# Performance work log

Hardware: AMD Instinct MI355X
Metric: run time of the kernel (lower is better)

The kernel has to match this reference:

```python
import jax, jax.numpy as jnp
import numpy as np

D = H = W = 128
NUM_STEPS = 7  # MONAI DVF2DDF default


def _base_grid(dtype):
    zz, yy, xx = jnp.meshgrid(jnp.arange(D, dtype=dtype),
                              jnp.arange(H, dtype=dtype),
                              jnp.arange(W, dtype=dtype), indexing='ij')
    return jnp.stack([zz, yy, xx], 0)  # [3,D,H,W] voxel coords


def _warp(img, ddf, mode):
    # img: [1,C,D,H,W], ddf: [1,3,D,H,W] in voxel units.
    # Equivalent to grid_sample(align_corners=True, padding='border'):
    # border padding == clamp the voxel-space sample coordinate to [0, dim-1].
    dtype = ddf.dtype
    coords = _base_grid(dtype) + ddf[0]
    lims = jnp.array([D - 1, H - 1, W - 1], dtype=dtype).reshape(3, 1, 1, 1)
    coords = jnp.clip(coords, 0.0, lims)
    vol = img[0]  # [C,D,H,W]
    if mode == 'nearest':
        zi, yi, xi = jnp.round(coords).astype(jnp.int32)
        return vol[:, zi, yi, xi][None]
    z, y, x = coords
    z0 = jnp.floor(z); y0 = jnp.floor(y); x0 = jnp.floor(x)
    wz = z - z0; wy = y - y0; wx = x - x0
    z0i = z0.astype(jnp.int32); y0i = y0.astype(jnp.int32); x0i = x0.astype(jnp.int32)
    z1i = jnp.minimum(z0i + 1, D - 1)
    y1i = jnp.minimum(y0i + 1, H - 1)
    x1i = jnp.minimum(x0i + 1, W - 1)
    g = lambda a, b, c: vol[:, a, b, c]  # [C,D,H,W] gather
    out = (g(z0i, y0i, x0i) * (1 - wz) * (1 - wy) * (1 - wx)
         + g(z0i, y0i, x1i) * (1 - wz) * (1 - wy) * wx
         + g(z0i, y1i, x0i) * (1 - wz) * wy * (1 - wx)
         + g(z0i, y1i, x1i) * (1 - wz) * wy * wx
         + g(z1i, y0i, x0i) * wz * (1 - wy) * (1 - wx)
         + g(z1i, y0i, x1i) * wz * (1 - wy) * wx
         + g(z1i, y1i, x0i) * wz * wy * (1 - wx)
         + g(z1i, y1i, x1i) * wz * wy * wx)
    return out[None]


def _dvf2ddf(dvf):
    # scaling-and-squaring integration of a stationary velocity field
    ddf = dvf / (2.0 ** NUM_STEPS)
    for _ in range(NUM_STEPS):
        ddf = ddf + _warp(ddf, ddf, 'bilinear')
    return ddf


def setup_inputs() -> dict:
    key = jax.random.key(0)
    k1, k2, k3, k4 = jax.random.split(key, 4)
    dvf = jax.random.normal(k1, (1, 3, D, H, W), dtype=jnp.float32) * 0.5
    moving_image = jax.random.uniform(k2, (1, 1, D, H, W), dtype=jnp.float32)
    fixed_image = jax.random.uniform(k3, (1, 1, D, H, W), dtype=jnp.float32)
    moving_label = jax.random.randint(k4, (1, 1, D, H, W), 0, 4).astype(jnp.float32)
    return {'dvf': dvf, 'moving_image': moving_image,
            'fixed_image': fixed_image, 'moving_label': moving_label}


def reference(dvf, moving_image, fixed_image, moving_label):
    ddf = _dvf2ddf(dvf)
    pred_image = _warp(moving_image, ddf, 'bilinear')
    pred_label = _warp(moving_label, ddf, 'nearest')
    return (ddf, pred_image, pred_label, dvf)
```

## Files before the change

### kernel.cpp

```cpp
#include <hip/hip_runtime.h>

#define DD 128
constexpr int NV = DD * DD * DD;
constexpr float SCALE = 1.0f / 128.0f;

__device__ __forceinline__ int swizzle_block(int b) {
    return (b & 7) * 1024 + (b >> 3);
}

__device__ __forceinline__ void unpack_zyx(int tid, int& z, int& y, int& x) {
    x = tid & (DD - 1);
    y = (tid >> 7) & (DD - 1);
    z = tid >> 14;
}

__device__ __forceinline__ float clampc(float v) {
    return fminf(fmaxf(v, 0.0f), (float)(DD - 1));
}

struct Corners {
    int i000, i001, i010, i011, i100, i101, i110, i111;
    float w000, w001, w010, w011, w100, w101, w110, w111;
};

__device__ __forceinline__ Corners corner_setup(float cz, float cy, float cx) {
    float z0f = floorf(cz), y0f = floorf(cy), x0f = floorf(cx);
    float wz = cz - z0f, wy = cy - y0f, wx = cx - x0f;
    int z0 = (int)z0f, y0 = (int)y0f, x0 = (int)x0f;
    int z1 = min(z0 + 1, DD - 1);
    int y1 = min(y0 + 1, DD - 1);
    int x1 = min(x0 + 1, DD - 1);
    float omz = 1.0f - wz, omy = 1.0f - wy, omx = 1.0f - wx;
    int zs0 = z0 << 14, zs1 = z1 << 14;
    int ys0 = y0 << 7,  ys1 = y1 << 7;
    Corners c;
    c.i000 = zs0 + ys0 + x0; c.i001 = zs0 + ys0 + x1;
    c.i010 = zs0 + ys1 + x0; c.i011 = zs0 + ys1 + x1;
    c.i100 = zs1 + ys0 + x0; c.i101 = zs1 + ys0 + x1;
    c.i110 = zs1 + ys1 + x0; c.i111 = zs1 + ys1 + x1;
    c.w000 = omz * omy * omx; c.w001 = omz * omy * wx;
    c.w010 = omz * wy * omx;  c.w011 = omz * wy * wx;
    c.w100 = wz * omy * omx;  c.w101 = wz * omy * wx;
    c.w110 = wz * wy * omx;   c.w111 = wz * wy * wx;
    return c;
}

__device__ __forceinline__ void trilerp3i(const float* __restrict__ src,
                                          const Corners& c,
                                          float& r0, float& r1, float& r2) {
    const float* p000 = src + 3 * c.i000; const float* p001 = src + 3 * c.i001;
    const float* p010 = src + 3 * c.i010; const float* p011 = src + 3 * c.i011;
    const float* p100 = src + 3 * c.i100; const float* p101 = src + 3 * c.i101;
    const float* p110 = src + 3 * c.i110; const float* p111 = src + 3 * c.i111;
    r0 = c.w000*p000[0] + c.w001*p001[0] + c.w010*p010[0] + c.w011*p011[0]
       + c.w100*p100[0] + c.w101*p101[0] + c.w110*p110[0] + c.w111*p111[0];
    r1 = c.w000*p000[1] + c.w001*p001[1] + c.w010*p010[1] + c.w011*p011[1]
       + c.w100*p100[1] + c.w101*p101[1] + c.w110*p110[1] + c.w111*p111[1];
    r2 = c.w000*p000[2] + c.w001*p001[2] + c.w010*p010[2] + c.w011*p011[2]
       + c.w100*p100[2] + c.w101*p101[2] + c.w110*p110[2] + c.w111*p111[2];
}

__global__ __launch_bounds__(256)
void step1_kernel(const float* __restrict__ dvf, float* __restrict__ dst) {
    int b = swizzle_block(blockIdx.x);
    int tid = b * 256 + threadIdx.x;
    int z, y, x;
    unpack_zyx(tid, z, y, x);

    float d0 = dvf[tid] * SCALE;
    float d1 = dvf[tid + NV] * SCALE;
    float d2 = dvf[tid + 2 * NV] * SCALE;

    Corners c = corner_setup(clampc((float)z + d0),
                             clampc((float)y + d1),
                             clampc((float)x + d2));

    float r0 = 0.f, r1 = 0.f, r2 = 0.f;
    {
        const float* s0 = dvf;
        const float* s1 = dvf + NV;
        const float* s2 = dvf + 2 * NV;
        r0 = c.w000*s0[c.i000] + c.w001*s0[c.i001] + c.w010*s0[c.i010] + c.w011*s0[c.i011]
           + c.w100*s0[c.i100] + c.w101*s0[c.i101] + c.w110*s0[c.i110] + c.w111*s0[c.i111];
        r1 = c.w000*s1[c.i000] + c.w001*s1[c.i001] + c.w010*s1[c.i010] + c.w011*s1[c.i011]
           + c.w100*s1[c.i100] + c.w101*s1[c.i101] + c.w110*s1[c.i110] + c.w111*s1[c.i111];
        r2 = c.w000*s2[c.i000] + c.w001*s2[c.i001] + c.w010*s2[c.i010] + c.w011*s2[c.i011]
           + c.w100*s2[c.i100] + c.w101*s2[c.i101] + c.w110*s2[c.i110] + c.w111*s2[c.i111];
    }

    float* p = dst + 3 * tid;
    p[0] = d0 + r0 * SCALE;
    p[1] = d1 + r1 * SCALE;
    p[2] = d2 + r2 * SCALE;
}

__global__ __launch_bounds__(256)
void step_kernel(const float* __restrict__ src, float* __restrict__ dst) {
    int b = swizzle_block(blockIdx.x);
    int tid = b * 256 + threadIdx.x;
    int z, y, x;
    unpack_zyx(tid, z, y, x);

    const float* s = src + 3 * tid;
    float d0 = s[0], d1 = s[1], d2 = s[2];

    Corners c = corner_setup(clampc((float)z + d0),
                             clampc((float)y + d1),
                             clampc((float)x + d2));
    float r0, r1, r2;
    trilerp3i(src, c, r0, r1, r2);

    float* p = dst + 3 * tid;
    p[0] = d0 + r0; p[1] = d1 + r1; p[2] = d2 + r2;
}

__global__ __launch_bounds__(256)
void step7_final_kernel(const float* __restrict__ src,
                        const float* __restrict__ mimg,
                        const float* __restrict__ mlab,
                        float* __restrict__ ddf_out,
                        float* __restrict__ pred_img,
                        float* __restrict__ pred_lab) {
    int b = swizzle_block(blockIdx.x);
    int tid = b * 256 + threadIdx.x;
    int z, y, x;
    unpack_zyx(tid, z, y, x);

    const float* s = src + 3 * tid;
    float d0 = s[0], d1 = s[1], d2 = s[2];

    Corners c = corner_setup(clampc((float)z + d0),
                             clampc((float)y + d1),
                             clampc((float)x + d2));
    float r0, r1, r2;
    trilerp3i(src, c, r0, r1, r2);

    r0 += d0; r1 += d1; r2 += d2;
    ddf_out[tid]          = r0;
    ddf_out[tid + NV]     = r1;
    ddf_out[tid + 2 * NV] = r2;

    float cz = clampc((float)z + r0);
    float cy = clampc((float)y + r1);
    float cx = clampc((float)x + r2);

    {
        Corners g = corner_setup(cz, cy, cx);
        float v = g.w000*mimg[g.i000] + g.w001*mimg[g.i001]
                + g.w010*mimg[g.i010] + g.w011*mimg[g.i011]
                + g.w100*mimg[g.i100] + g.w101*mimg[g.i101]
                + g.w110*mimg[g.i110] + g.w111*mimg[g.i111];
        pred_img[tid] = v;
    }
    {
        int zi = (int)rintf(cz);
        int yi = (int)rintf(cy);
        int xi = (int)rintf(cx);
        pred_lab[tid] = mlab[(zi << 14) + (yi << 7) + xi];
    }
}

__global__ __launch_bounds__(256)
void copy_dvf_kernel(const float4* __restrict__ dvf, float4* __restrict__ dvf_out) {
    int tid = blockIdx.x * blockDim.x + threadIdx.x;
    dvf_out[tid] = dvf[tid];
}

extern "C" void kernel_launch(void* const* d_in, const int* in_sizes, int n_in,
                              void* d_out, int out_size, void* d_ws, size_t ws_size,
                              hipStream_t stream) {
    const float* dvf  = (const float*)d_in[0];
    const float* mimg = (const float*)d_in[1];
    const float* mlab = (const float*)d_in[3];

    float* out      = (float*)d_out;
    float* ddf_out  = out;
    float* pred_img = out + 3 * NV;
    float* pred_lab = out + 4 * NV;
    float* dvf_out  = out + 5 * NV;

    float* A = dvf_out;
    float* B = ddf_out;

    dim3 block(256);
    dim3 grid(NV / 256);

    step1_kernel<<<grid, block, 0, stream>>>(dvf, B);
    step_kernel<<<grid, block, 0, stream>>>(B, A);
    step_kernel<<<grid, block, 0, stream>>>(A, B);
    step_kernel<<<grid, block, 0, stream>>>(B, A);
    step_kernel<<<grid, block, 0, stream>>>(A, B);
    step_kernel<<<grid, block, 0, stream>>>(B, A);
    step7_final_kernel<<<grid, block, 0, stream>>>(A, mimg, mlab,
                                                   ddf_out, pred_img, pred_lab);
    copy_dvf_kernel<<<3 * NV / (4 * 256), block, 0, stream>>>(
        (const float4*)dvf, (float4*)dvf_out);
}
```

Before: 267.8 us.

## Pad displacement field to float4 for single-load vectorized trilinear gathers

```diff
diff --git a/kernel.cpp b/kernel.cpp
--- a/kernel.cpp
+++ b/kernel.cpp
@@ -3,10 +3,6 @@
 #define DD 128
 constexpr int NV = DD * DD * DD;
 constexpr float SCALE = 1.0f / 128.0f;
-
-__device__ __forceinline__ int swizzle_block(int b) {
-    return (b & 7) * 1024 + (b >> 3);
-}
 
 __device__ __forceinline__ void unpack_zyx(int tid, int& z, int& y, int& x) {
     x = tid & (DD - 1);
@@ -45,6 +41,105 @@
     return c;
 }
 
+
+__global__ __launch_bounds__(256)
+void pack_kernel(const float* __restrict__ dvf, float4* __restrict__ dst) {
+    int tid = blockIdx.x * blockDim.x + threadIdx.x;
+    float4 v;
+    v.x = dvf[tid] * SCALE;
+    v.y = dvf[tid + NV] * SCALE;
+    v.z = dvf[tid + 2 * NV] * SCALE;
+    v.w = 0.0f;
+    dst[tid] = v;
+}
+
+__global__ __launch_bounds__(256)
+void step4_kernel(const float4* __restrict__ src, float4* __restrict__ dst) {
+    int tid = blockIdx.x * blockDim.x + threadIdx.x;
+    int z, y, x;
+    unpack_zyx(tid, z, y, x);
+
+    float4 s = src[tid];
+
+    Corners c = corner_setup(clampc((float)z + s.x),
+                             clampc((float)y + s.y),
+                             clampc((float)x + s.z));
+
+    float4 v000 = src[c.i000], v001 = src[c.i001];
+    float4 v010 = src[c.i010], v011 = src[c.i011];
+    float4 v100 = src[c.i100], v101 = src[c.i101];
+    float4 v110 = src[c.i110], v111 = src[c.i111];
+
+    float4 r;
+    r.x = s.x + c.w000*v000.x + c.w001*v001.x + c.w010*v010.x + c.w011*v011.x
+              + c.w100*v100.x + c.w101*v101.x + c.w110*v110.x + c.w111*v111.x;
+    r.y = s.y + c.w000*v000.y + c.w001*v001.y + c.w010*v010.y + c.w011*v011.y
+              + c.w100*v100.y + c.w101*v101.y + c.w110*v110.y + c.w111*v111.y;
+    r.z = s.z + c.w000*v000.z + c.w001*v001.z + c.w010*v010.z + c.w011*v011.z
+              + c.w100*v100.z + c.w101*v101.z + c.w110*v110.z + c.w111*v111.z;
+    r.w = 0.0f;
+    dst[tid] = r;
+}
+
+__global__ __launch_bounds__(256)
+void step7_final4_kernel(const float4* __restrict__ src,
+                         const float* __restrict__ mimg,
+                         const float* __restrict__ mlab,
+                         float* __restrict__ ddf_out,
+                         float* __restrict__ pred_img,
+                         float* __restrict__ pred_lab) {
+    int tid = blockIdx.x * blockDim.x + threadIdx.x;
+    int z, y, x;
+    unpack_zyx(tid, z, y, x);
+
+    float4 s = src[tid];
+
+    Corners c = corner_setup(clampc((float)z + s.x),
+                             clampc((float)y + s.y),
+                             clampc((float)x + s.z));
+
+    float4 v000 = src[c.i000], v001 = src[c.i001];
+    float4 v010 = src[c.i010], v011 = src[c.i011];
+    float4 v100 = src[c.i100], v101 = src[c.i101];
+    float4 v110 = src[c.i110], v111 = src[c.i111];
+
+    float r0 = s.x + c.w000*v000.x + c.w001*v001.x + c.w010*v010.x + c.w011*v011.x
+                   + c.w100*v100.x + c.w101*v101.x + c.w110*v110.x + c.w111*v111.x;
+    float r1 = s.y + c.w000*v000.y + c.w001*v001.y + c.w010*v010.y + c.w011*v011.y
+                   + c.w100*v100.y + c.w101*v101.y + c.w110*v110.y + c.w111*v111.y;
+    float r2 = s.z + c.w000*v000.z + c.w001*v001.z + c.w010*v010.z + c.w011*v011.z
+                   + c.w100*v100.z + c.w101*v101.z + c.w110*v110.z + c.w111*v111.z;
+
+    ddf_out[tid]          = r0;
+    ddf_out[tid + NV]     = r1;
+    ddf_out[tid + 2 * NV] = r2;
+
+    float cz = clampc((float)z + r0);
+    float cy = clampc((float)y + r1);
+    float cx = clampc((float)x + r2);
+
+    {
+        Corners g = corner_setup(cz, cy, cx);
+        pred_img[tid] = g.w000*mimg[g.i000] + g.w001*mimg[g.i001]
+                      + g.w010*mimg[g.i010] + g.w011*mimg[g.i011]
+                      + g.w100*mimg[g.i100] + g.w101*mimg[g.i101]
+                      + g.w110*mimg[g.i110] + g.w111*mimg[g.i111];
+    }
+    {
+        int zi = (int)rintf(cz);
+        int yi = (int)rintf(cy);
+        int xi = (int)rintf(cx);
+        pred_lab[tid] = mlab[(zi << 14) + (yi << 7) + xi];
+    }
+}
+
+__global__ __launch_bounds__(256)
+void copy_dvf_kernel(const float4* __restrict__ dvf, float4* __restrict__ dvf_out) {
+    int tid = blockIdx.x * blockDim.x + threadIdx.x;
+    dvf_out[tid] = dvf[tid];
+}
+
+
 __device__ __forceinline__ void trilerp3i(const float* __restrict__ src,
                                           const Corners& c,
                                           float& r0, float& r1, float& r2) {
@@ -61,96 +156,60 @@
 }
 
 __global__ __launch_bounds__(256)
-void step1_kernel(const float* __restrict__ dvf, float* __restrict__ dst) {
-    int b = swizzle_block(blockIdx.x);
-    int tid = b * 256 + threadIdx.x;
-    int z, y, x;
-    unpack_zyx(tid, z, y, x);
-
-    float d0 = dvf[tid] * SCALE;
-    float d1 = dvf[tid + NV] * SCALE;
-    float d2 = dvf[tid + 2 * NV] * SCALE;
-
-    Corners c = corner_setup(clampc((float)z + d0),
-                             clampc((float)y + d1),
-                             clampc((float)x + d2));
-
-    float r0 = 0.f, r1 = 0.f, r2 = 0.f;
-    {
-        const float* s0 = dvf;
-        const float* s1 = dvf + NV;
-        const float* s2 = dvf + 2 * NV;
-        r0 = c.w000*s0[c.i000] + c.w001*s0[c.i001] + c.w010*s0[c.i010] + c.w011*s0[c.i011]
-           + c.w100*s0[c.i100] + c.w101*s0[c.i101] + c.w110*s0[c.i110] + c.w111*s0[c.i111];
-        r1 = c.w000*s1[c.i000] + c.w001*s1[c.i001] + c.w010*s1[c.i010] + c.w011*s1[c.i011]
-           + c.w100*s1[c.i100] + c.w101*s1[c.i101] + c.w110*s1[c.i110] + c.w111*s1[c.i111];
-        r2 = c.w000*s2[c.i000] + c.w001*s2[c.i001] + c.w010*s2[c.i010] + c.w011*s2[c.i011]
-           + c.w100*s2[c.i100] + c.w101*s2[c.i101] + c.w110*s2[c.i110] + c.w111*s2[c.i111];
-    }
-
-    float* p = dst + 3 * tid;
-    p[0] = d0 + r0 * SCALE;
-    p[1] = d1 + r1 * SCALE;
-    p[2] = d2 + r2 * SCALE;
-}
-
-__global__ __launch_bounds__(256)
-void step_kernel(const float* __restrict__ src, float* __restrict__ dst) {
-    int b = swizzle_block(blockIdx.x);
-    int tid = b * 256 + threadIdx.x;
-    int z, y, x;
-    unpack_zyx(tid, z, y, x);
-
+void init3_kernel(const float* __restrict__ dvf, float* __restrict__ A) {
+    int tid = blockIdx.x * blockDim.x + threadIdx.x;
+    float* p = A + 3 * tid;
+    p[0] = dvf[tid] * SCALE;
+    p[1] = dvf[tid + NV] * SCALE;
+    p[2] = dvf[tid + 2 * NV] * SCALE;
+}
+
+__global__ __launch_bounds__(256)
+void step3_kernel(const float* __restrict__ src, float* __restrict__ dst) {
+    int tid = blockIdx.x * blockDim.x + threadIdx.x;
+    int z, y, x;
+    unpack_zyx(tid, z, y, x);
     const float* s = src + 3 * tid;
     float d0 = s[0], d1 = s[1], d2 = s[2];
-
     Corners c = corner_setup(clampc((float)z + d0),
                              clampc((float)y + d1),
                              clampc((float)x + d2));
     float r0, r1, r2;
     trilerp3i(src, c, r0, r1, r2);
-
     float* p = dst + 3 * tid;
     p[0] = d0 + r0; p[1] = d1 + r1; p[2] = d2 + r2;
 }
 
 __global__ __launch_bounds__(256)
-void step7_final_kernel(const float* __restrict__ src,
-                        const float* __restrict__ mimg,
-                        const float* __restrict__ mlab,
-                        float* __restrict__ ddf_out,
-                        float* __restrict__ pred_img,
-                        float* __restrict__ pred_lab) {
-    int b = swizzle_block(blockIdx.x);
-    int tid = b * 256 + threadIdx.x;
-    int z, y, x;
-    unpack_zyx(tid, z, y, x);
-
+void step7_final3_kernel(const float* __restrict__ src,
+                         const float* __restrict__ mimg,
+                         const float* __restrict__ mlab,
+                         float* __restrict__ ddf_out,
+                         float* __restrict__ pred_img,
+                         float* __restrict__ pred_lab) {
+    int tid = blockIdx.x * blockDim.x + threadIdx.x;
+    int z, y, x;
+    unpack_zyx(tid, z, y, x);
     const float* s = src + 3 * tid;
     float d0 = s[0], d1 = s[1], d2 = s[2];
-
     Corners c = corner_setup(clampc((float)z + d0),
                              clampc((float)y + d1),
                              clampc((float)x + d2));
     float r0, r1, r2;
     trilerp3i(src, c, r0, r1, r2);
-
     r0 += d0; r1 += d1; r2 += d2;
     ddf_out[tid]          = r0;
     ddf_out[tid + NV]     = r1;
     ddf_out[tid + 2 * NV] = r2;
-
     float cz = clampc((float)z + r0);
     float cy = clampc((float)y + r1);
     float cx = clampc((float)x + r2);
-
     {
         Corners g = corner_setup(cz, cy, cx);
-        float v = g.w000*mimg[g.i000] + g.w001*mimg[g.i001]
-                + g.w010*mimg[g.i010] + g.w011*mimg[g.i011]
-                + g.w100*mimg[g.i100] + g.w101*mimg[g.i101]
-                + g.w110*mimg[g.i110] + g.w111*mimg[g.i111];
-        pred_img[tid] = v;
+        pred_img[tid] = g.w000*mimg[g.i000] + g.w001*mimg[g.i001]
+                      + g.w010*mimg[g.i010] + g.w011*mimg[g.i011]
+                      + g.w100*mimg[g.i100] + g.w101*mimg[g.i101]
+                      + g.w110*mimg[g.i110] + g.w111*mimg[g.i111];
     }
     {
         int zi = (int)rintf(cz);
@@ -160,11 +219,6 @@
     }
 }
 
-__global__ __launch_bounds__(256)
-void copy_dvf_kernel(const float4* __restrict__ dvf, float4* __restrict__ dvf_out) {
-    int tid = blockIdx.x * blockDim.x + threadIdx.x;
-    dvf_out[tid] = dvf[tid];
-}
 
 extern "C" void kernel_launch(void* const* d_in, const int* in_sizes, int n_in,
                               void* d_out, int out_size, void* d_ws, size_t ws_size,
@@ -179,20 +233,37 @@
     float* pred_lab = out + 4 * NV;
     float* dvf_out  = out + 5 * NV;
 
-    float* A = dvf_out;
-    float* B = ddf_out;
-
     dim3 block(256);
     dim3 grid(NV / 256);
 
-    step1_kernel<<<grid, block, 0, stream>>>(dvf, B);
-    step_kernel<<<grid, block, 0, stream>>>(B, A);
-    step_kernel<<<grid, block, 0, stream>>>(A, B);
-    step_kernel<<<grid, block, 0, stream>>>(B, A);
-    step_kernel<<<grid, block, 0, stream>>>(A, B);
-    step_kernel<<<grid, block, 0, stream>>>(B, A);
-    step7_final_kernel<<<grid, block, 0, stream>>>(A, mimg, mlab,
-                                                   ddf_out, pred_img, pred_lab);
-    copy_dvf_kernel<<<3 * NV / (4 * 256), block, 0, stream>>>(
-        (const float4*)dvf, (float4*)dvf_out);
-}
+    if (ws_size >= (size_t)NV * 4 * sizeof(float)) {
+        float4* P = (float4*)d_ws;
+        float4* Q = (float4*)(out + 4 * NV);
+
+        pack_kernel<<<grid, block, 0, stream>>>(dvf, P);
+        step4_kernel<<<grid, block, 0, stream>>>(P, Q);
+        step4_kernel<<<grid, block, 0, stream>>>(Q, P);
+        step4_kernel<<<grid, block, 0, stream>>>(P, Q);
+        step4_kernel<<<grid, block, 0, stream>>>(Q, P);
+        step4_kernel<<<grid, block, 0, stream>>>(P, Q);
+        step4_kernel<<<grid, block, 0, stream>>>(Q, P);
+        step7_final4_kernel<<<grid, block, 0, stream>>>(P, mimg, mlab,
+                                                        ddf_out, pred_img, pred_lab);
+        copy_dvf_kernel<<<3 * NV / (4 * 256), block, 0, stream>>>(
+            (const float4*)dvf, (float4*)dvf_out);
+    } else {
+        float* A = dvf_out;
+        float* B = ddf_out;
+        init3_kernel<<<grid, block, 0, stream>>>(dvf, A);
+        step3_kernel<<<grid, block, 0, stream>>>(A, B);
+        step3_kernel<<<grid, block, 0, stream>>>(B, A);
+        step3_kernel<<<grid, block, 0, stream>>>(A, B);
+        step3_kernel<<<grid, block, 0, stream>>>(B, A);
+        step3_kernel<<<grid, block, 0, stream>>>(A, B);
+        step3_kernel<<<grid, block, 0, stream>>>(B, A);
+        step7_final3_kernel<<<grid, block, 0, stream>>>(A, mimg, mlab,
+                                                        ddf_out, pred_img, pred_lab);
+        copy_dvf_kernel<<<3 * NV / (4 * 256), block, 0, stream>>>(
+            (const float4*)dvf, (float4*)dvf_out);
+    }
+}
```

Result: slower. 284.9 us (+6.4%).
